# Performance work log

Hardware: AMD Instinct MI355X
Metric: run time of the kernel (lower is better)

The kernel has to match this reference:

```python
import jax, jax.numpy as jnp
import numpy as np

STRIDE = 4
EPS = 1e-12  # guards sqrt grad at exactly-zero distance (weight[0] is all zeros)


def rbf_conv(x, w, stride=STRIDE):
    # x: (N, 1, H, W); w: (O, kh, kw). Computes per-window cdist to all O
    # prototype filters, then gauss RBF with std = unbiased std of the (N, O)
    # distance matrix at each window position (matches torch.std(dist)).
    O, kh, kw = w.shape
    patches = jax.lax.conv_general_dilated_patches(
        x, (kh, kw), (stride, stride), 'VALID')      # (N, kh*kw, oh, ow)
    p = jnp.transpose(patches, (0, 2, 3, 1))          # (N, oh, ow, P)
    wf = w.reshape(O, -1)                              # (O, P)
    d2 = (jnp.sum(p * p, -1)[..., None] + jnp.sum(wf * wf, -1)
          - 2.0 * jnp.einsum('nhwp,op->nhwo', p, wf))
    dist = jnp.sqrt(jnp.maximum(d2, 0.0) + EPS)       # (N, oh, ow, O)
    std = jnp.std(dist, axis=(0, 3), ddof=1, keepdims=True)  # per window pos
    out = jnp.exp(-0.5 * (dist / std) ** 2)           # gauss RBF
    return jnp.transpose(out, (0, 3, 1, 2))           # (N, O, oh, ow)


def crelu(x, b):
    return x * (x >= b).astype(x.dtype)


def sfm(x, shape, next_kernel, filt, alpha0=0.9):
    # get_RM: (N, C, h_in, w_in) -> (B, h, w, C) regrouping, then alpha-weighted
    # patch pooling over `filt`, emitting (B*h'*w', 1, kh_next, kw_next).
    h, w = shape
    f0, f1 = filt
    C = x.shape[1]
    rm = jnp.transpose(x, (0, 2, 3, 1)).reshape(-1, h, w, C)
    seq = jnp.arange(f0 * f1, dtype=x.dtype)[::-1]       # flipped sequence
    alpha = jnp.tile((alpha0 ** seq).reshape(f0, f1), (h // f0, w // f1))
    out = rm * alpha[None, :, :, None]
    out = out.reshape(-1, h // f0, f0, w // f1, f1, C).mean(axis=(2, 4))
    return out.reshape(-1, 1, *next_kernel)


def channel_forward(xc, w1, w2, w3, w4, cb):
    y = rbf_conv(xc, w1)                       # (B, 100, 6, 6)
    y = crelu(y, cb[0])
    y = sfm(y, (6, 6), (10, 10), (2, 2))       # (B*9, 1, 10, 10)
    y = rbf_conv(y, w2)                        # (B*9, 225, 1, 1)
    y = crelu(y, cb[1])
    y = sfm(y, (3, 3), (15, 15), (1, 3))       # (B*3, 1, 15, 15)
    y = rbf_conv(y, w3)                        # (B*3, 625, 1, 1)
    y = crelu(y, cb[2])
    y = sfm(y, (3, 1), (25, 25), (3, 1))       # (B, 1, 25, 25)
    y = rbf_conv(y, w4)                        # (B, 1225, 1, 1)
    y = crelu(y, cb[3])
    return y


def forward(x, w1, w2, w3, w4, fc_w, fc_b, crelu_bias):
    B = x.shape[0]
    feats = [channel_forward(x[:, c:c + 1], w1[c], w2[c], w3[c], w4[c], crelu_bias)
             for c in range(x.shape[1])]        # fixed loop over 3 color channels
    out = jnp.concatenate(feats, axis=1).reshape(B, -1)  # (B, 3*1225)
    return out @ fc_w.T + fc_b


def setup_inputs() -> dict:
    key = jax.random.key(0)
    ks = jax.random.split(key, 8)

    def kaiming_u(k, shape):
        fan_in = int(np.prod(shape[2:]))        # 1*kh*kw, matches torch
        bound = float(np.sqrt(1.0 / fan_in))    # kaiming_uniform(a=sqrt(5))
        w = jax.random.uniform(k, shape, jnp.float32, -bound, bound)
        return w.at[:, 0].set(0.0)              # torch init zeros filter 0

    B = 4096
    return {
        'x': jax.random.uniform(ks[0], (B, 3, 28, 28), jnp.float32),
        'w1': kaiming_u(ks[1], (3, 100, 5, 5)),
        'w2': kaiming_u(ks[2], (3, 225, 10, 10)),
        'w3': kaiming_u(ks[3], (3, 625, 15, 15)),
        'w4': kaiming_u(ks[4], (3, 1225, 25, 25)),
        'fc_w': jax.random.normal(ks[5], (10, 3 * 1225), jnp.float32) * 0.016,
        'fc_b': jnp.zeros((10,), jnp.float32),
        'crelu_bias': jnp.array([0.4, 0.1, 0.01, 0.01], jnp.float32),
    }


def reference(x, w1, w2, w3, w4, fc_w, fc_b, crelu_bias):
    return forward(x, w1, w2, w3, w4, fc_w, fc_b, crelu_bias)
```

## Files before the change

### kernel.cpp

```cpp
#include <hip/hip_runtime.h>


typedef unsigned short u16;
typedef short bf16x8 __attribute__((ext_vector_type(8)));
typedef float f32x4 __attribute__((ext_vector_type(4)));

#define STRIPES 64
#define ACC_L2 0
#define ACC_L3 128
#define ACC_L4 256
#define ACC_TOTAL 384

__device__ __forceinline__ u16 f2bf(float f) {
  unsigned int u = __float_as_uint(f);
  unsigned int r = (u + 0x7fffu + ((u >> 16) & 1u)) >> 16;
  return (u16)r;
}
__device__ __forceinline__ float bf2f(u16 h) {
  return __uint_as_float(((unsigned int)h) << 16);
}
__device__ __forceinline__ float fexp(float x) { return __expf(x); }
__device__ __forceinline__ float fsqrt(float x) { return __builtin_amdgcn_sqrtf(x); }
__device__ __forceinline__ void gload16(const void* g, const void* l) {
  __builtin_amdgcn_global_load_lds(
      (const __attribute__((address_space(1))) unsigned int*)g,
      (__attribute__((address_space(3))) unsigned int*)l, 16, 0, 0);
}

__global__ void zero_acc_kernel(double* __restrict__ acc, int n) {
  int i = blockIdx.x * blockDim.x + threadIdx.x;
  if (i < n) acc[i] = 0.0;
}

__global__ __launch_bounds__(128) void w_prep(
    const float* __restrict__ W, int O, int K, int Opad, int Kp,
    u16* __restrict__ hi, u16* __restrict__ lo, float* __restrict__ wn)
{
  __shared__ float red[2];
  int o = blockIdx.x, cc = blockIdx.y, t = threadIdx.x;
  const float* src = W + ((size_t)cc * O + o) * K;
  u16* dh = hi + ((size_t)cc * Opad + o) * Kp;
  u16* dl = lo + ((size_t)cc * Opad + o) * Kp;
  float p = 0.f;
  for (int k = t; k < Kp; k += 128) {
    float v = (o < O && k < K) ? src[k] : 0.f;
    u16 h = f2bf(v);
    u16 l = f2bf(v - bf2f(h));
    dh[k] = h; dl[k] = l;
    p = fmaf(v, v, p);
  }
  for (int off = 32; off; off >>= 1) p += __shfl_down(p, off, 64);
  if ((t & 63) == 0) red[t >> 6] = p;
  __syncthreads();
  if (t == 0) wn[(size_t)cc * Opad + o] = red[0] + red[1];
}

__global__ __launch_bounds__(256) void l1_gemm_d2(
    const float* __restrict__ x, int c0,
    const u16* __restrict__ W1h, const u16* __restrict__ W1l,
    const float* __restrict__ w1n, float* __restrict__ dist1, int sD1c)
{
  __shared__ __align__(16) u16 sm[16384];
  __shared__ float img[1568];
  __shared__ float pnsm[512];
  __shared__ float pnloc[128];
  const int t = threadIdx.x;
  const int w = t >> 6, lane = t & 63;
  const int b0 = blockIdx.x * 2;
  const int zi = blockIdx.y, c = c0 + zi;
  const u16* Wh = W1h + (size_t)c * 4096;
  const u16* Wl = W1l + (size_t)c * 4096;
  const float* wn = w1n + (size_t)c * 128;
  dist1 += (size_t)zi * sD1c;

  {
    const int kk = (w & 3) * 8;
#pragma unroll
    for (int u = 0; u < 2; ++u) {
      const size_t gb = (size_t)(u * 64 + lane) * 32 + kk;
      const int ls = ((w & 3) * 128 + u * 64) * 8;
      gload16(Wh + gb, sm + 8192 + ls);
      gload16(Wl + gb, sm + 12288 + ls);
    }
  }
#pragma unroll
  for (int im = 0; im < 2; ++im) {
    if (t < 196)
      ((float4*)(img + im * 784))[t] =
          ((const float4*)(x + ((size_t)(b0 + im) * 3 + c) * 784))[t];
  }
  __syncthreads();
  for (int s = t; s < 512; s += 256) {
    int q = s >> 7, row = s & 127;
    int im = row >> 6, pr = row & 63;
    int pi = pr / 6, pj = pr - pi * 6;
    const float* ib = img + im * 784 + pi * 4 * 28 + pj * 4;
    float v[8]; float pn = 0.f;
#pragma unroll
    for (int e = 0; e < 8; ++e) {
      int k = q * 8 + e;
      float val = 0.f;
      if (pr < 36 && k < 25) { int r = k / 5, ss = k - r * 5; val = ib[r * 28 + ss]; }
      v[e] = val; pn = fmaf(val, val, pn);
    }
    u16 hi8[8], lo8[8];
#pragma unroll
    for (int e = 0; e < 8; ++e) {
      u16 h = f2bf(v[e]); hi8[e] = h; lo8[e] = f2bf(v[e] - bf2f(h));
    }
    *(bf16x8*)(sm + (q * 128 + row) * 8) = *(bf16x8*)hi8;
    *(bf16x8*)(sm + 4096 + (q * 128 + row) * 8) = *(bf16x8*)lo8;
    pnsm[s] = pn;
  }
  asm volatile("s_waitcnt vmcnt(0)" ::: "memory");
  __syncthreads();
  if (t < 128) pnloc[t] = pnsm[t] + pnsm[128 + t] + pnsm[256 + t] + pnsm[384 + t];

  const int wr = w >> 1, wc = w & 1;
  const int q4 = lane >> 4, r16 = lane & 15;
  f32x4 accv[4][4];
#pragma unroll
  for (int i = 0; i < 4; ++i)
#pragma unroll
    for (int j = 0; j < 4; ++j) accv[i][j] = (f32x4){0.f, 0.f, 0.f, 0.f};

  bf16x8 Ah[4], Al[4], Bh[4], Bl[4];
#pragma unroll
  for (int i = 0; i < 4; ++i) {
    int ao = (q4 * 128 + wr * 64 + i * 16 + r16) * 8;
    int bo = (q4 * 128 + wc * 64 + i * 16 + r16) * 8;
    Ah[i] = *(const bf16x8*)(sm + ao);
    Al[i] = *(const bf16x8*)(sm + 4096 + ao);
    Bh[i] = *(const bf16x8*)(sm + 8192 + bo);
    Bl[i] = *(const bf16x8*)(sm + 12288 + bo);
  }
#pragma unroll
  for (int j = 0; j < 4; ++j) {
#pragma unroll
    for (int i = 0; i < 4; ++i)
      accv[i][j] = __builtin_amdgcn_mfma_f32_16x16x32_bf16(Ah[i], Bh[j], accv[i][j], 0, 0, 0);
#pragma unroll
    for (int i = 0; i < 4; ++i)
      accv[i][j] = __builtin_amdgcn_mfma_f32_16x16x32_bf16(Al[i], Bh[j], accv[i][j], 0, 0, 0);
#pragma unroll
    for (int i = 0; i < 4; ++i)
      accv[i][j] = __builtin_amdgcn_mfma_f32_16x16x32_bf16(Ah[i], Bl[j], accv[i][j], 0, 0, 0);
  }
  __syncthreads();

  int colv[4]; float wnv[4];
#pragma unroll
  for (int j = 0; j < 4; ++j) {
    colv[j] = wc * 64 + j * 16 + r16;
    wnv[j] = (colv[j] < 100) ? wn[colv[j]] : 0.f;
  }
#pragma unroll
  for (int i = 0; i < 4; ++i) {
#pragma unroll
    for (int r = 0; r < 4; ++r) {
      int pos = i * 16 + q4 * 4 + r;
      if (pos < 36) {
        float pn = pnloc[wr * 64 + pos];
        float* drow = dist1 + ((size_t)(b0 + wr) * 36 + pos) * 100;
#pragma unroll
        for (int j = 0; j < 4; ++j) {
          if (colv[j] < 100) {
            float d2 = pn + wnv[j] - 2.f * accv[i][j][r];
            drow[colv[j]] = fmaxf(d2, 0.f) + 1e-12f;
          }
        }
      }
    }
  }
}

__global__ __launch_bounds__(256) void l1_reduce_bw(
    const float* __restrict__ d1, int sD1c, int B, float* __restrict__ part, int sPartc)
{
  __shared__ float sh[8];
  int pos = blockIdx.x, stripe = blockIdx.y, zi = blockIdx.z, t = threadIdx.x;
  d1 += (size_t)zi * sD1c; part += (size_t)zi * sPartc;
  int ch = t & 127, bsub = t >> 7;
  float s = 0.f, q = 0.f;
  if (ch < 100) {
    int nb = B / 64;
    for (int bi = bsub; bi < nb; bi += 2) {
      float v = d1[((size_t)(bi * 64 + stripe) * 36 + pos) * 100 + ch];
      s += fsqrt(v); q += v;
    }
  }
  for (int off = 32; off; off >>= 1) {
    s += __shfl_down(s, off, 64);
    q += __shfl_down(q, off, 64);
  }
  if ((t & 63) == 0) { sh[(t >> 6) * 2] = s; sh[(t >> 6) * 2 + 1] = q; }
  __syncthreads();
  if (t == 0) {
    s = sh[0] + sh[2] + sh[4] + sh[6];
    q = sh[1] + sh[3] + sh[5] + sh[7];
    part[pos * STRIPES + stripe] = s;
    part[(36 + pos) * STRIPES + stripe] = q;
  }
}

__global__ __launch_bounds__(256) void l1_part_fin(
    const float* __restrict__ part, int sPartc, float* __restrict__ inv36, int sInvc,
    double n)
{
  __shared__ double sh[8];
  int pos = blockIdx.x, zi = blockIdx.y, t = threadIdx.x;
  part += (size_t)zi * sPartc; inv36 += (size_t)zi * sInvc;
  double s = 0.0, q = 0.0;
  for (int b = t; b < STRIPES; b += 256) {
    s += part[(size_t)pos * STRIPES + b];
    q += part[(size_t)(36 + pos) * STRIPES + b];
  }
  for (int off = 32; off; off >>= 1) {
    s += __shfl_down(s, off, 64);
    q += __shfl_down(q, off, 64);
  }
  if ((t & 63) == 0) { sh[(t >> 6) * 2] = s; sh[(t >> 6) * 2 + 1] = q; }
  __syncthreads();
  if (t == 0) {
    s = sh[0] + sh[2] + sh[4] + sh[6];
    q = sh[1] + sh[3] + sh[5] + sh[7];
    double var = (q - s * s / n) / (n - 1.0);
    inv36[pos] = var > 0.0 ? (float)(0.5 / var) : __builtin_inff();
  }
}

__global__ __launch_bounds__(128) void l1_sfm_lite(
    const float* __restrict__ d1, int sD1c,
    const float* __restrict__ inv36, int sInvc, const float* __restrict__ cb,
    u16* __restrict__ Xhi, u16* __restrict__ Xlo, float* __restrict__ xn,
    int sXc, int sxnc)
{
  __shared__ float inv_s[36];
  __shared__ float xnsm[9][2];
  int b = blockIdx.x, zi = blockIdx.y, t = threadIdx.x;
  d1 += (size_t)zi * sD1c; inv36 += (size_t)zi * sInvc;
  Xhi += (size_t)zi * sXc; Xlo += (size_t)zi * sXc; xn += (size_t)zi * sxnc;
  if (t < 36) inv_s[t] = inv36[t];
  __syncthreads();
  const float* db = d1 + (size_t)b * 3600;
  float bias = cb[0];
  int wv = t >> 6;
#pragma unroll
  for (int IJ = 0; IJ < 9; ++IJ) {
    const int I = IJ / 3, J = IJ - I * 3;
    const int p00 = 12 * I + 2 * J;
    float v = 0.f;
    if (t < 100) {
      float e00 = fexp(-db[p00 * 100 + t] * inv_s[p00]);
      float e01 = fexp(-db[(p00 + 1) * 100 + t] * inv_s[p00 + 1]);
      float e10 = fexp(-db[(p00 + 6) * 100 + t] * inv_s[p00 + 6]);
      float e11 = fexp(-db[(p00 + 7) * 100 + t] * inv_s[p00 + 7]);
      e00 = (e00 >= bias) ? e00 : 0.f;
      e01 = (e01 >= bias) ? e01 : 0.f;
      e10 = (e10 >= bias) ? e10 : 0.f;
      e11 = (e11 >= bias) ? e11 : 0.f;
      v = 0.25f * (fmaf(0.729f, e00, 0.81f * e01) + fmaf(0.9f, e10, e11));
    }
    size_t xrow = (size_t)b * 9 + IJ;
    u16 h = f2bf(v);
    u16 l = f2bf(v - bf2f(h));
    Xhi[xrow * 128 + t] = h;
    Xlo[xrow * 128 + t] = l;
    float p = v * v;
    for (int off = 32; off; off >>= 1) p += __shfl_down(p, off, 64);
    if ((t & 63) == 0) xnsm[IJ][wv] = p;
  }
  __syncthreads();
  if (t < 9) xn[(size_t)b * 9 + t] = xnsm[t][0] + xnsm[t][1];
}

__global__ __launch_bounds__(512, 2) void gemm_dist_pipe(
    const u16* __restrict__ Xhi, const u16* __restrict__ Xlo,
    const u16* __restrict__ Whi, const u16* __restrict__ Wlo,
    const float* __restrict__ xn, const float* __restrict__ wn,
    float* __restrict__ dist, int O, int Kp,
    double* __restrict__ acc, int accbase, int c0,
    int sXc, int sWc, int sxnc, int swnc, int sdistc)
{
  __shared__ __align__(16) u16 sm[65536];
  int zi = blockIdx.z, c = c0 + zi;
  Xhi += (size_t)zi * sXc; Xlo += (size_t)zi * sXc;
  Whi += (size_t)c * sWc;  Wlo += (size_t)c * sWc;
  xn += (size_t)zi * sxnc; wn += (size_t)c * swnc;
  dist += (size_t)zi * sdistc;
  acc += (size_t)c * ACC_TOTAL;

  const int t = threadIdx.x;
  const int w = t >> 6, lane = t & 63;
  const int wr = w >> 1, wc = w & 1;
  const int sq = w & 3, half = w >> 2;
  const int m0 = blockIdx.x * 256, o0 = blockIdx.y * 256;
  const int q4 = lane >> 4, r16 = lane & 15;
  const int nsteps = Kp / 32;

  f32x4 accv[4][8];
#pragma unroll
  for (int i = 0; i < 4; ++i)
#pragma unroll
    for (int j = 0; j < 8; ++j) accv[i][j] = (f32x4){0.f, 0.f, 0.f, 0.f};

  auto stage = [&](int buf, int ks) {
    const int kk = ks * 32 + sq * 8;
    u16* base = sm + buf * 32768;
#pragma unroll
    for (int u = 0; u < 2; ++u) {
      const int row = half * 128 + u * 64 + lane;
      const size_t ga = (size_t)(m0 + row) * Kp + kk;
      const size_t gb = (size_t)(o0 + row) * Kp + kk;
      const int ls = (sq * 256 + half * 128 + u * 64) * 8;
      gload16(Xhi + ga, base + ls);
      gload16(Xlo + ga, base + 8192 + ls);
      gload16(Whi + gb, base + 16384 + ls);
      gload16(Wlo + gb, base + 24576 + ls);
    }
  };

  stage(0, 0);
  for (int ks = 0; ks < nsteps; ++ks) {
    asm volatile("s_waitcnt vmcnt(0)\n\ts_barrier" ::: "memory");
    if (ks + 1 < nsteps) stage((ks + 1) & 1, ks + 1);
    const u16* base = sm + (ks & 1) * 32768;

    bf16x8 Ah[4], Al[4];
#pragma unroll
    for (int i = 0; i < 4; ++i) {
      int ao = (q4 * 256 + wr * 64 + i * 16 + r16) * 8;
      Ah[i] = *(const bf16x8*)(base + ao);
      Al[i] = *(const bf16x8*)(base + 8192 + ao);
    }
#pragma unroll
    for (int j = 0; j < 8; ++j) {
      int bo = (q4 * 256 + wc * 128 + j * 16 + r16) * 8;
      bf16x8 Bh = *(const bf16x8*)(base + 16384 + bo);
      bf16x8 Bl = *(const bf16x8*)(base + 24576 + bo);
#pragma unroll
      for (int i = 0; i < 4; ++i)
        accv[i][j] = __builtin_amdgcn_mfma_f32_16x16x32_bf16(Ah[i], Bh, accv[i][j], 0, 0, 0);
#pragma unroll
      for (int i = 0; i < 4; ++i)
        accv[i][j] = __builtin_amdgcn_mfma_f32_16x16x32_bf16(Al[i], Bh, accv[i][j], 0, 0, 0);
#pragma unroll
      for (int i = 0; i < 4; ++i)
        accv[i][j] = __builtin_amdgcn_mfma_f32_16x16x32_bf16(Ah[i], Bl, accv[i][j], 0, 0, 0);
    }
    asm volatile("s_barrier" ::: "memory");
  }

  double s = 0.0, qd = 0.0;
#pragma unroll
  for (int i = 0; i < 4; ++i) {
    const int mb = m0 + wr * 64 + i * 16 + q4 * 4;
    float xnv[4];
#pragma unroll
    for (int r = 0; r < 4; ++r) xnv[r] = xn[mb + r];
    float sf = 0.f, qf = 0.f;
#pragma unroll
    for (int j = 0; j < 8; ++j) {
      const int o = o0 + wc * 128 + j * 16 + r16;
      if (o < O) {
        const float wnv = wn[o];
#pragma unroll
        for (int r = 0; r < 4; ++r) {
          float d2 = xnv[r] + wnv - 2.f * accv[i][j][r];
          float d2c = fmaxf(d2, 0.f) + 1e-12f;
          dist[(size_t)(mb + r) * O + o] = d2c;
          sf += fsqrt(d2c); qf += d2c;
        }
      }
    }
    s += sf; qd += qf;
  }
  for (int off = 32; off; off >>= 1) {
    s += __shfl_down(s, off, 64);
    qd += __shfl_down(qd, off, 64);
  }
  double* redsm = (double*)sm;
  if (lane == 0) { redsm[w * 2] = s; redsm[w * 2 + 1] = qd; }
  __syncthreads();
  if (t == 0) {
    s = 0.0; qd = 0.0;
#pragma unroll
    for (int ww = 0; ww < 8; ++ww) { s += redsm[ww * 2]; qd += redsm[ww * 2 + 1]; }
    int stripe = (blockIdx.x + blockIdx.y * gridDim.x) & (STRIPES - 1);
    atomicAdd(&acc[accbase + stripe * 2], s);
    atomicAdd(&acc[accbase + stripe * 2 + 1], qd);
  }
}

__device__ __forceinline__ float block_inv_from_acc(
    const double* __restrict__ acc, int base, double n, float* sh)
{
  __syncthreads();
  int t = threadIdx.x;
  if (t < 64) {
    double s = acc[base + 2 * t], q = acc[base + 2 * t + 1];
    for (int off = 32; off; off >>= 1) {
      s += __shfl_down(s, off, 64);
      q += __shfl_down(q, off, 64);
    }
    if (t == 0) {
      double var = (q - s * s / n) / (n - 1.0);
      *sh = var > 0.0 ? (float)(0.5 / var) : __builtin_inff();
    }
  }
  __syncthreads();
  return *sh;
}

__global__ __launch_bounds__(256) void l2_sfm(
    const float* __restrict__ dist2, const double* __restrict__ acc, double n,
    const float* __restrict__ cb, u16* __restrict__ Xhi, u16* __restrict__ Xlo,
    float* __restrict__ xn, int c0, int sdistc, int sXc, int sxnc)
{
  __shared__ float shinv;
  __shared__ float red[4];
  int zi = blockIdx.z, c = c0 + zi;
  dist2 += (size_t)zi * sdistc;
  Xhi += (size_t)zi * sXc; Xlo += (size_t)zi * sXc; xn += (size_t)zi * sxnc;
  float inv = block_inv_from_acc(acc + (size_t)c * ACC_TOTAL, ACC_L2, n, &shinv);
  int b = blockIdx.x, u = blockIdx.y, ch = threadIdx.x;
  float bias = cb[1];
  float v = 0.f;
  if (ch < 225) {
    const float av[3] = {0.81f, 0.9f, 1.0f};
    float a = 0.f;
#pragma unroll
    for (int vv = 0; vv < 3; ++vv) {
      float d2 = dist2[((size_t)b * 9 + u * 3 + vv) * 225 + ch];
      float e = fexp(-d2 * inv);
      e = (e >= bias) ? e : 0.f;
      a = fmaf(e, av[vv], a);
    }
    v = a * (1.f / 3.f);
  }
  size_t row = (size_t)b * 3 + u;
  u16 h = f2bf(v);
  u16 l = f2bf(v - bf2f(h));
  Xhi[row * 256 + ch] = h;
  Xlo[row * 256 + ch] = l;
  float p = v * v;
  for (int off = 32; off; off >>= 1) p += __shfl_down(p, off, 64);
  if ((ch & 63) == 0) red[ch >> 6] = p;
  __syncthreads();
  if (ch == 0) xn[row] = red[0] + red[1] + red[2] + red[3];
}

__global__ __launch_bounds__(256) void l3_sfm(
    const float* __restrict__ dist3, const double* __restrict__ acc, double n,
    const float* __restrict__ cb, u16* __restrict__ Xhi, u16* __restrict__ Xlo,
    float* __restrict__ xn, int c0, int sdistc, int sXc, int sxnc)
{
  __shared__ float shinv;
  __shared__ float red[4];
  int zi = blockIdx.y, c = c0 + zi;
  dist3 += (size_t)zi * sdistc;
  Xhi += (size_t)zi * sXc; Xlo += (size_t)zi * sXc; xn += (size_t)zi * sxnc;
  float inv = block_inv_from_acc(acc + (size_t)c * ACC_TOTAL, ACC_L3, n, &shinv);
  int b = blockIdx.x, t = threadIdx.x;
  float bias = cb[2];
  const float au[3] = {0.81f, 0.9f, 1.0f};
  float p = 0.f;
  for (int ch = t; ch < 640; ch += 256) {
    float v = 0.f;
    if (ch < 625) {
      float a = 0.f;
#pragma unroll
      for (int u = 0; u < 3; ++u) {
        float d2 = dist3[((size_t)b * 3 + u) * 625 + ch];
        float e = fexp(-d2 * inv);
        e = (e >= bias) ? e : 0.f;
        a = fmaf(e, au[u], a);
      }
      v = a * (1.f / 3.f);
    }
    u16 h = f2bf(v);
    u16 l = f2bf(v - bf2f(h));
    Xhi[(size_t)b * 640 + ch] = h;
    Xlo[(size_t)b * 640 + ch] = l;
    p = fmaf(v, v, p);
  }
  for (int off = 32; off; off >>= 1) p += __shfl_down(p, off, 64);
  if ((t & 63) == 0) red[t >> 6] = p;
  __syncthreads();
  if (t == 0) xn[b] = red[0] + red[1] + red[2] + red[3];
}

__global__ __launch_bounds__(128) void fc_acc(
    const float* __restrict__ dist4, const double* __restrict__ acc, double n,
    const float* __restrict__ cb, const float* __restrict__ fcw,
    const float* __restrict__ fcb, float* __restrict__ out,
    int c0, int nc, int sdistc)
{
  __shared__ float shinv;
  int b = blockIdx.x, t = threadIdx.x;
  float bias = cb[3];
  float p[10];
#pragma unroll
  for (int k = 0; k < 10; ++k) p[k] = 0.f;
  for (int zi = 0; zi < nc; ++zi) {
    int c = c0 + zi;
    float inv = block_inv_from_acc(acc + (size_t)c * ACC_TOTAL, ACC_L4, n, &shinv);
    const float* d4 = dist4 + (size_t)zi * sdistc;
    for (int j = t; j < 1225; j += 128) {
      float d2 = d4[(size_t)b * 1225 + j];
      float v = fexp(-d2 * inv);
      v = (v >= bias) ? v : 0.f;
#pragma unroll
      for (int k = 0; k < 10; ++k) p[k] = fmaf(v, fcw[k * 3675 + c * 1225 + j], p[k]);
    }
  }
#pragma unroll
  for (int k = 0; k < 10; ++k)
    for (int off = 32; off; off >>= 1) p[k] += __shfl_down(p[k], off, 64);
  __shared__ float red[2][10];
  int wave = t >> 6;
  if ((t & 63) == 0) {
#pragma unroll
    for (int k = 0; k < 10; ++k) red[wave][k] = p[k];
  }
  __syncthreads();
  if (t < 10) {
    float v = red[0][t] + red[1][t];
    if (c0 == 0) out[(size_t)b * 10 + t] = fcb[t] + v;
    else         out[(size_t)b * 10 + t] += v;
  }
}

extern "C" void kernel_launch(void* const* d_in, const int* in_sizes, int n_in,
                              void* d_out, int out_size, void* d_ws, size_t ws_size,
                              hipStream_t stream) {
  const float* x   = (const float*)d_in[0];
  const float* w1  = (const float*)d_in[1];
  const float* w2  = (const float*)d_in[2];
  const float* w3  = (const float*)d_in[3];
  const float* w4  = (const float*)d_in[4];
  const float* fcw = (const float*)d_in[5];
  const float* fcb = (const float*)d_in[6];
  const float* cb  = (const float*)d_in[7];
  float* out = (float*)d_out;
  const int B = in_sizes[0] / (3 * 28 * 28);
  const int M2 = B * 9, M3 = B * 3;
  const int NB = B / 2;

  const size_t W2SZ = 256 * 128, W3SZ = 768 * 256, W4SZ = (size_t)1280 * 640;
  const size_t WTOT = 3 * (W2SZ + W3SZ + W4SZ);

  int tier;
  u16 *Xbase, *Whi, *Wlo, *W1h, *W1l;
  float *wn, *w1n, *xn, *inv36, *part;
  double* accd;
  float* Sf;
  for (tier = 0; tier < 3; ++tier) {
    size_t cur = 0;
    char* basep = (char*)d_ws;
    auto take = [&](size_t bytes) {
      void* r = basep + cur;
      cur = (cur + bytes + 255) & ~(size_t)255;
      return r;
    };
    int nc = (tier <= 1) ? 3 : 1;
    int ncL1 = (tier == 0) ? 3 : 1;
    size_t Ssz = (size_t)M2 * 225 * 4 * nc;
    size_t d1sz = (size_t)B * 3600 * 4 * ncL1;
    if (d1sz > Ssz) Ssz = d1sz;
    Sf = (float*)take(Ssz);
    Xbase = (u16*)take((size_t)M2 * 128 * 2 * 2 * nc);
    Whi = (u16*)take(WTOT * 2); Wlo = (u16*)take(WTOT * 2);
    W1h = (u16*)take(12288 * 2); W1l = (u16*)take(12288 * 2);
    wn  = (float*)take(3 * (256 + 768 + 1280) * 4);
    w1n = (float*)take(384 * 4);
    xn    = (float*)take((size_t)M2 * 4 * nc);
    inv36 = (float*)take(40 * 4 * ncL1);
    part  = (float*)take((size_t)72 * STRIPES * 4 * ncL1);
    accd  = (double*)take(3 * ACC_TOTAL * 8);
    if (cur <= ws_size || tier == 2) break;
  }
  const int nc = (tier <= 1) ? 3 : 1;
  const bool batL1 = (tier == 0);

  const int sX2c   = (nc == 3) ? M2 * 128 * 2 : 0;
  const int sX3c   = (nc == 3) ? M3 * 256 * 2 : 0;
  const int sX4c   = (nc == 3) ? B * 640 * 2 : 0;
  const int sD2c   = (nc == 3) ? M2 * 225 : 0;
  const int sD3c   = (nc == 3) ? M3 * 625 : 0;
  const int sD4c   = (nc == 3) ? B * 1225 : 0;
  const int sXn2c  = (nc == 3) ? M2 : 0;
  const int sXn3c  = (nc == 3) ? M3 : 0;
  const int sXn4c  = (nc == 3) ? B : 0;
  const int sD1c   = batL1 ? B * 3600 : 0;
  const int sPartc = batL1 ? 72 * STRIPES : 0;
  const int sInvL1 = batL1 ? 40 : 0;

  u16* x2hi = Xbase;   u16* x2lo = Xbase + (size_t)M2 * 128;
  u16* x3hi = Xbase;   u16* x3lo = Xbase + (size_t)M3 * 256;
  u16* x4hi = Xbase;   u16* x4lo = Xbase + (size_t)B * 640;
  u16* Whi2 = Whi;                 u16* Wlo2 = Wlo;                 float* wn2 = wn;
  u16* Whi3 = Whi + 3 * W2SZ;      u16* Wlo3 = Wlo + 3 * W2SZ;      float* wn3 = wn + 3 * 256;
  u16* Whi4 = Whi + 3 * (W2SZ + W3SZ); u16* Wlo4 = Wlo + 3 * (W2SZ + W3SZ);
  float* wn4 = wn + 3 * (256 + 768);

  zero_acc_kernel<<<(3 * ACC_TOTAL + 255) / 256, 256, 0, stream>>>(accd, 3 * ACC_TOTAL);
  w_prep<<<dim3(128, 3),  128, 0, stream>>>(w1, 100, 25,  128, 32,  W1h,  W1l,  w1n);
  w_prep<<<dim3(256, 3),  128, 0, stream>>>(w2, 225, 100, 256, 128, Whi2, Wlo2, wn2);
  w_prep<<<dim3(768, 3),  128, 0, stream>>>(w3, 625, 225, 768, 256, Whi3, Wlo3, wn3);
  w_prep<<<dim3(1280, 3), 128, 0, stream>>>(w4, 1225, 625, 1280, 640, Whi4, Wlo4, wn4);

  for (int c0 = 0; c0 < 3; c0 += nc) {
    if (batL1) {
      l1_gemm_d2<<<dim3(NB, 3), 256, 0, stream>>>(x, 0, W1h, W1l, w1n, Sf, sD1c);
      l1_reduce_bw<<<dim3(36, STRIPES, 3), 256, 0, stream>>>(Sf, sD1c, B, part, sPartc);
      l1_part_fin<<<dim3(36, 3), 256, 0, stream>>>(part, sPartc, inv36, sInvL1,
                                                   (double)B * 100.0);
      l1_sfm_lite<<<dim3(B, 3), 128, 0, stream>>>(
          Sf, sD1c, inv36, sInvL1, cb, x2hi, x2lo, xn, sX2c, sXn2c);
    } else {
      for (int ci = 0; ci < nc; ++ci) {
        int c = c0 + ci;
        l1_gemm_d2<<<dim3(NB, 1), 256, 0, stream>>>(x, c, W1h, W1l, w1n, Sf, 0);
        l1_reduce_bw<<<dim3(36, STRIPES, 1), 256, 0, stream>>>(Sf, 0, B, part, 0);
        l1_part_fin<<<dim3(36, 1), 256, 0, stream>>>(part, 0, inv36, 0,
                                                     (double)B * 100.0);
        l1_sfm_lite<<<dim3(B, 1), 128, 0, stream>>>(
            Sf, 0, inv36, 0, cb, x2hi + (size_t)ci * sX2c, x2lo + (size_t)ci * sX2c,
            xn + (size_t)ci * sXn2c, 0, 0);
      }
    }

    gemm_dist_pipe<<<dim3(M2 / 256, 1, nc), 512, 0, stream>>>(
        x2hi, x2lo, Whi2, Wlo2, xn, wn2, Sf, 225, 128, accd, ACC_L2, c0,
        sX2c, (int)W2SZ, sXn2c, 256, sD2c);
    l2_sfm<<<dim3(B, 3, nc), 256, 0, stream>>>(
        Sf, accd, (double)M2 * 225.0, cb, x3hi, x3lo, xn, c0, sD2c, sX3c, sXn3c);

    gemm_dist_pipe<<<dim3(M3 / 256, 3, nc), 512, 0, stream>>>(
        x3hi, x3lo, Whi3, Wlo3, xn, wn3, Sf, 625, 256, accd, ACC_L3, c0,
        sX3c, (int)W3SZ, sXn3c, 768, sD3c);
    l3_sfm<<<dim3(B, nc), 256, 0, stream>>>(
        Sf, accd, (double)M3 * 625.0, cb, x4hi, x4lo, xn, c0, sD3c, sX4c, sXn4c);

    gemm_dist_pipe<<<dim3(B / 256, 5, nc), 512, 0, stream>>>(
        x4hi, x4lo, Whi4, Wlo4, xn, wn4, Sf, 1225, 640, accd, ACC_L4, c0,
        sX4c, (int)W4SZ, sXn4c, 1280, sD4c);
    fc_acc<<<B, 128, 0, stream>>>(
        Sf, accd, (double)B * 1225.0, cb, fcw, fcb, out, c0, nc, sD4c);
  }
}
```

Before: 528.3 us.

## Fuse layer-1 distance statistics into GEMM and split-stage the distance GEMM pipeline

The layer-1 sum and sum-of-squares reduction of sqrt-distances now happens in the l1_gemm_d2 epilogue. Each block writes per-position partials, so the separate l1_reduce_bw kernel and its full re-read of the distance buffer are gone, and l1_part_fin now reduces over NB blocks instead of 64 stripes. Separately, the main distance GEMM splits staging into A and B halves with partial vmcnt waits, two barriers per k-step and s_setprio around the MFMA sections, so the next tile's loads overlap the current compute. The cost is more partials to finalize and more barriers per k-step.

```diff
diff --git a/kernel.cpp b/kernel.cpp
--- a/kernel.cpp
+++ b/kernel.cpp
@@ -58,12 +58,14 @@
 __global__ __launch_bounds__(256) void l1_gemm_d2(
     const float* __restrict__ x, int c0,
     const u16* __restrict__ W1h, const u16* __restrict__ W1l,
-    const float* __restrict__ w1n, float* __restrict__ dist1, int sD1c)
+    const float* __restrict__ w1n, float* __restrict__ dist1, int sD1c,
+    float* __restrict__ part, int sPartc, int NBLK)
 {
   __shared__ __align__(16) u16 sm[16384];
   __shared__ float img[1568];
   __shared__ float pnsm[512];
   __shared__ float pnloc[128];
+  __shared__ float sqred[4][36][2];
   const int t = threadIdx.x;
   const int w = t >> 6, lane = t & 63;
   const int b0 = blockIdx.x * 2;
@@ -72,6 +74,7 @@
   const u16* Wl = W1l + (size_t)c * 4096;
   const float* wn = w1n + (size_t)c * 128;
   dist1 += (size_t)zi * sD1c;
+  part  += (size_t)zi * sPartc;
 
   {
     const int kk = (w & 3) * 8;
@@ -162,58 +165,45 @@
       if (pos < 36) {
         float pn = pnloc[wr * 64 + pos];
         float* drow = dist1 + ((size_t)(b0 + wr) * 36 + pos) * 100;
+        float sl = 0.f, ql = 0.f;
 #pragma unroll
         for (int j = 0; j < 4; ++j) {
           if (colv[j] < 100) {
             float d2 = pn + wnv[j] - 2.f * accv[i][j][r];
-            drow[colv[j]] = fmaxf(d2, 0.f) + 1e-12f;
+            float d2c = fmaxf(d2, 0.f) + 1e-12f;
+            drow[colv[j]] = d2c;
+            sl += fsqrt(d2c); ql += d2c;
           }
         }
+#pragma unroll
+        for (int off = 8; off; off >>= 1) {
+          sl += __shfl_xor(sl, off, 64);
+          ql += __shfl_xor(ql, off, 64);
+        }
+        if (r16 == 0) { sqred[w][pos][0] = sl; sqred[w][pos][1] = ql; }
       }
     }
   }
-}
-
-__global__ __launch_bounds__(256) void l1_reduce_bw(
-    const float* __restrict__ d1, int sD1c, int B, float* __restrict__ part, int sPartc)
-{
-  __shared__ float sh[8];
-  int pos = blockIdx.x, stripe = blockIdx.y, zi = blockIdx.z, t = threadIdx.x;
-  d1 += (size_t)zi * sD1c; part += (size_t)zi * sPartc;
-  int ch = t & 127, bsub = t >> 7;
-  float s = 0.f, q = 0.f;
-  if (ch < 100) {
-    int nb = B / 64;
-    for (int bi = bsub; bi < nb; bi += 2) {
-      float v = d1[((size_t)(bi * 64 + stripe) * 36 + pos) * 100 + ch];
-      s += fsqrt(v); q += v;
-    }
-  }
-  for (int off = 32; off; off >>= 1) {
-    s += __shfl_down(s, off, 64);
-    q += __shfl_down(q, off, 64);
-  }
-  if ((t & 63) == 0) { sh[(t >> 6) * 2] = s; sh[(t >> 6) * 2 + 1] = q; }
-  __syncthreads();
-  if (t == 0) {
-    s = sh[0] + sh[2] + sh[4] + sh[6];
-    q = sh[1] + sh[3] + sh[5] + sh[7];
-    part[pos * STRIPES + stripe] = s;
-    part[(36 + pos) * STRIPES + stripe] = q;
+  __syncthreads();
+  if (t < 36) {
+    float ss = sqred[0][t][0] + sqred[1][t][0] + sqred[2][t][0] + sqred[3][t][0];
+    float qq = sqred[0][t][1] + sqred[1][t][1] + sqred[2][t][1] + sqred[3][t][1];
+    part[(size_t)t * NBLK + blockIdx.x] = ss;
+    part[(size_t)(36 + t) * NBLK + blockIdx.x] = qq;
   }
 }
 
 __global__ __launch_bounds__(256) void l1_part_fin(
     const float* __restrict__ part, int sPartc, float* __restrict__ inv36, int sInvc,
-    double n)
+    double n, int NBLK)
 {
   __shared__ double sh[8];
   int pos = blockIdx.x, zi = blockIdx.y, t = threadIdx.x;
   part += (size_t)zi * sPartc; inv36 += (size_t)zi * sInvc;
   double s = 0.0, q = 0.0;
-  for (int b = t; b < STRIPES; b += 256) {
-    s += part[(size_t)pos * STRIPES + b];
-    q += part[(size_t)(36 + pos) * STRIPES + b];
+  for (int b = t; b < NBLK; b += 256) {
+    s += part[(size_t)pos * NBLK + b];
+    q += part[(size_t)(36 + pos) * NBLK + b];
   }
   for (int off = 32; off; off >>= 1) {
     s += __shfl_down(s, off, 64);
@@ -304,27 +294,37 @@
 #pragma unroll
     for (int j = 0; j < 8; ++j) accv[i][j] = (f32x4){0.f, 0.f, 0.f, 0.f};
 
-  auto stage = [&](int buf, int ks) {
+  auto stageA = [&](int buf, int ks) {
     const int kk = ks * 32 + sq * 8;
     u16* base = sm + buf * 32768;
 #pragma unroll
     for (int u = 0; u < 2; ++u) {
       const int row = half * 128 + u * 64 + lane;
       const size_t ga = (size_t)(m0 + row) * Kp + kk;
-      const size_t gb = (size_t)(o0 + row) * Kp + kk;
       const int ls = (sq * 256 + half * 128 + u * 64) * 8;
       gload16(Xhi + ga, base + ls);
       gload16(Xlo + ga, base + 8192 + ls);
+    }
+  };
+  auto stageB = [&](int buf, int ks) {
+    const int kk = ks * 32 + sq * 8;
+    u16* base = sm + buf * 32768;
+#pragma unroll
+    for (int u = 0; u < 2; ++u) {
+      const int row = half * 128 + u * 64 + lane;
+      const size_t gb = (size_t)(o0 + row) * Kp + kk;
+      const int ls = (sq * 256 + half * 128 + u * 64) * 8;
       gload16(Whi + gb, base + 16384 + ls);
       gload16(Wlo + gb, base + 24576 + ls);
     }
   };
 
-  stage(0, 0);
+  stageA(0, 0);
+  stageB(0, 0);
   for (int ks = 0; ks < nsteps; ++ks) {
-    asm volatile("s_waitcnt vmcnt(0)\n\ts_barrier" ::: "memory");
-    if (ks + 1 < nsteps) stage((ks + 1) & 1, ks + 1);
     const u16* base = sm + (ks & 1) * 32768;
+    asm volatile("s_waitcnt vmcnt(2)\n\ts_barrier" ::: "memory");
+    if (ks + 1 < nsteps) stageA((ks + 1) & 1, ks + 1);
 
     bf16x8 Ah[4], Al[4];
 #pragma unroll
@@ -333,8 +333,9 @@
       Ah[i] = *(const bf16x8*)(base + ao);
       Al[i] = *(const bf16x8*)(base + 8192 + ao);
     }
-#pragma unroll
-    for (int j = 0; j < 8; ++j) {
+    __builtin_amdgcn_s_setprio(1);
+#pragma unroll
+    for (int j = 0; j < 4; ++j) {
       int bo = (q4 * 256 + wc * 128 + j * 16 + r16) * 8;
       bf16x8 Bh = *(const bf16x8*)(base + 16384 + bo);
       bf16x8 Bl = *(const bf16x8*)(base + 24576 + bo);
@@ -348,7 +349,31 @@
       for (int i = 0; i < 4; ++i)
         accv[i][j] = __builtin_amdgcn_mfma_f32_16x16x32_bf16(Ah[i], Bl, accv[i][j], 0, 0, 0);
     }
-    asm volatile("s_barrier" ::: "memory");
+    __builtin_amdgcn_s_setprio(0);
+
+    if (ks + 1 < nsteps) {
+      asm volatile("s_waitcnt vmcnt(4)\n\ts_barrier" ::: "memory");
+      stageB((ks + 1) & 1, ks + 1);
+    } else {
+      asm volatile("s_waitcnt vmcnt(0)\n\ts_barrier" ::: "memory");
+    }
+    __builtin_amdgcn_s_setprio(1);
+#pragma unroll
+    for (int j = 4; j < 8; ++j) {
+      int bo = (q4 * 256 + wc * 128 + j * 16 + r16) * 8;
+      bf16x8 Bh = *(const bf16x8*)(base + 16384 + bo);
+      bf16x8 Bl = *(const bf16x8*)(base + 24576 + bo);
+#pragma unroll
+      for (int i = 0; i < 4; ++i)
+        accv[i][j] = __builtin_amdgcn_mfma_f32_16x16x32_bf16(Ah[i], Bh, accv[i][j], 0, 0, 0);
+#pragma unroll
+      for (int i = 0; i < 4; ++i)
+        accv[i][j] = __builtin_amdgcn_mfma_f32_16x16x32_bf16(Al[i], Bh, accv[i][j], 0, 0, 0);
+#pragma unroll
+      for (int i = 0; i < 4; ++i)
+        accv[i][j] = __builtin_amdgcn_mfma_f32_16x16x32_bf16(Ah[i], Bl, accv[i][j], 0, 0, 0);
+    }
+    __builtin_amdgcn_s_setprio(0);
   }
 
   double s = 0.0, qd = 0.0;
@@ -379,7 +404,7 @@
     s += __shfl_down(s, off, 64);
     qd += __shfl_down(qd, off, 64);
   }
-  double* redsm = (double*)sm;
+  double* redsm = (double*)(sm + (nsteps & 1) * 32768);
   if (lane == 0) { redsm[w * 2] = s; redsm[w * 2 + 1] = qd; }
   __syncthreads();
   if (t == 0) {
@@ -576,7 +601,7 @@
     w1n = (float*)take(384 * 4);
     xn    = (float*)take((size_t)M2 * 4 * nc);
     inv36 = (float*)take(40 * 4 * ncL1);
-    part  = (float*)take((size_t)72 * STRIPES * 4 * ncL1);
+    part  = (float*)take((size_t)72 * NB * 4 * ncL1);
     accd  = (double*)take(3 * ACC_TOTAL * 8);
     if (cur <= ws_size || tier == 2) break;
   }
@@ -593,7 +618,7 @@
   const int sXn3c  = (nc == 3) ? M3 : 0;
   const int sXn4c  = (nc == 3) ? B : 0;
   const int sD1c   = batL1 ? B * 3600 : 0;
-  const int sPartc = batL1 ? 72 * STRIPES : 0;
+  const int sPartc = batL1 ? 72 * NB : 0;
   const int sInvL1 = batL1 ? 40 : 0;
 
   u16* x2hi = Xbase;   u16* x2lo = Xbase + (size_t)M2 * 128;
@@ -612,19 +637,19 @@
 
   for (int c0 = 0; c0 < 3; c0 += nc) {
     if (batL1) {
-      l1_gemm_d2<<<dim3(NB, 3), 256, 0, stream>>>(x, 0, W1h, W1l, w1n, Sf, sD1c);
-      l1_reduce_bw<<<dim3(36, STRIPES, 3), 256, 0, stream>>>(Sf, sD1c, B, part, sPartc);
+      l1_gemm_d2<<<dim3(NB, 3), 256, 0, stream>>>(x, 0, W1h, W1l, w1n, Sf, sD1c,
+                                                  part, sPartc, NB);
       l1_part_fin<<<dim3(36, 3), 256, 0, stream>>>(part, sPartc, inv36, sInvL1,
-                                                   (double)B * 100.0);
+                                                   (double)B * 100.0, NB);
       l1_sfm_lite<<<dim3(B, 3), 128, 0, stream>>>(
           Sf, sD1c, inv36, sInvL1, cb, x2hi, x2lo, xn, sX2c, sXn2c);
     } else {
       for (int ci = 0; ci < nc; ++ci) {
         int c = c0 + ci;
-        l1_gemm_d2<<<dim3(NB, 1), 256, 0, stream>>>(x, c, W1h, W1l, w1n, Sf, 0);
-        l1_reduce_bw<<<dim3(36, STRIPES, 1), 256, 0, stream>>>(Sf, 0, B, part, 0);
+        l1_gemm_d2<<<dim3(NB, 1), 256, 0, stream>>>(x, c, W1h, W1l, w1n, Sf, 0,
+                                                    part, 0, NB);
         l1_part_fin<<<dim3(36, 1), 256, 0, stream>>>(part, 0, inv36, 0,
-                                                     (double)B * 100.0);
+                                                     (double)B * 100.0, NB);
         l1_sfm_lite<<<dim3(B, 1), 128, 0, stream>>>(
             Sf, 0, inv36, 0, cb, x2hi + (size_t)ci * sX2c, x2lo + (size_t)ci * sX2c,
             xn + (size_t)ci * sXn2c, 0, 0);
```

Measured after the change: 490.9 us. 1.08x faster.
